# Kernel tuning notes

Hardware: AMD Instinct MI355X
Metric: run time of the kernel (lower is better)

Reference implementation:

```python
import jax, jax.numpy as jnp
import numpy as np

B, N, F_IN = 8, 1024, 256
N_HEADS, N_HIDDEN = 8, 32  # out_features=256, is_concat=True -> n_hidden = 256//8
NEG_SLOPE = 0.2


def setup_inputs() -> dict:
    key = jax.random.key(0)
    k1, k2, k3 = jax.random.split(key, 3)
    vertex = jax.random.normal(k1, (B, N, F_IN), dtype=jnp.float32)
    # linear_vert.weight.T  (applied as x @ w_vert)
    w_vert = jax.random.normal(k2, (F_IN, N_HEADS * N_HIDDEN), dtype=jnp.float32) / np.sqrt(F_IN)
    # attn linear: [2*n_hidden] -> 1, no bias; shared across heads
    attn_w = jax.random.normal(k3, (2 * N_HIDDEN,), dtype=jnp.float32) / np.sqrt(2 * N_HIDDEN)
    return {"vertex": vertex, "w_vert": w_vert, "attn_w": attn_w}


def reference(vertex, w_vert, attn_w):
    b, n, _ = vertex.shape
    # g_vertex: [b, n, h, d]
    g = jnp.einsum("bni,io->bno", vertex, w_vert).reshape(b, n, N_HEADS, N_HIDDEN)
    # attn(cat([g_i, g_j])) == g_i . w_src + g_j . w_dst  (cat index i = repeat_interleave half)
    w_src, w_dst = attn_w[:N_HIDDEN], attn_w[N_HIDDEN:]
    s_src = jnp.einsum("bnhd,d->bnh", g, w_src)  # [b, n, h]
    s_dst = jnp.einsum("bnhd,d->bnh", g, w_dst)  # [b, n, h]
    # e[b,i,j,h] = LeakyReLU(s_src[b,i,h] + s_dst[b,j,h])
    e = s_src[:, :, None, :] + s_dst[:, None, :, :]
    e = jnp.where(e >= 0, e, NEG_SLOPE * e)
    # softmax over j (dim=-2 after squeeze in the torch code)
    a = jax.nn.softmax(e, axis=2)  # [b, i, j, h]
    # dropout in eval mode = identity
    out = jnp.einsum("bijh,bjhd->bihd", a, g)  # [b, n, h, d]
    return out.reshape(b, n, N_HEADS * N_HIDDEN)
```

## Files before the change

### kernel.cpp

```cpp
#include <hip/hip_runtime.h>
#include <hip/hip_bf16.h>
#include <math.h>

#define F_IN  256
#define NOUT  256
#define NB    8
#define NN    1024
#define NH    8
#define ND    32
#define NROWS (NB * NN)
#define LOG2E 1.44269504f

typedef __attribute__((ext_vector_type(8))) short bf16x8;
typedef __attribute__((ext_vector_type(4))) float f32x4;

__device__ inline unsigned pk_bf16(float a, float b) {
    union { __hip_bfloat162 h2; unsigned u; } c;
    c.h2 = __float22bfloat162_rn(make_float2(a, b));
    return c.u;
}
__device__ inline unsigned short bf16u(float a) {
    union { __hip_bfloat16 h; unsigned short u; } c;
    c.h = __float2bfloat16(a);
    return c.u;
}
__device__ inline float bf2f(unsigned short u) {
    union { unsigned u; float f; } c;
    c.u = ((unsigned)u) << 16;
    return c.f;
}
__device__ inline void split8(const float4 va, const float4 vb,
                              bf16x8& hi, bf16x8& lo) {
    float f[8] = {va.x, va.y, va.z, va.w, vb.x, vb.y, vb.z, vb.w};
    union { bf16x8 v; unsigned u[4]; } H, L;
    #pragma unroll
    for (int i = 0; i < 4; ++i) {
        unsigned short h0 = bf16u(f[2 * i]);
        unsigned short h1 = bf16u(f[2 * i + 1]);
        H.u[i] = (unsigned)h0 | ((unsigned)h1 << 16);
        L.u[i] = pk_bf16(f[2 * i] - bf2f(h0), f[2 * i + 1] - bf2f(h1));
    }
    hi = H.v; lo = L.v;
}

__global__ __launch_bounds__(256) void w_prep_kernel(
    const float* __restrict__ w_vert,
    unsigned short* __restrict__ wT_hi, unsigned short* __restrict__ wT_lo)
{
    __shared__ float wf[64][68];
    const int t  = threadIdx.x;
    const int kt = (blockIdx.x >> 2) * 64;
    const int nt = (blockIdx.x & 3) * 64;
    #pragma unroll
    for (int q = 0; q < 4; ++q) {
        const int kr = (t >> 4) + 16 * q;
        const int nc = (t & 15) * 4;
        float4 v = *(const float4*)&w_vert[(size_t)(kt + kr) * NOUT + nt + nc];
        wf[kr][nc + 0] = v.x; wf[kr][nc + 1] = v.y;
        wf[kr][nc + 2] = v.z; wf[kr][nc + 3] = v.w;
    }
    __syncthreads();
    const int n = t >> 2, ks = (t & 3) * 16;
    union { unsigned u[8]; } Hs, Ls;
    #pragma unroll
    for (int i = 0; i < 8; ++i) {
        float x0 = wf[ks + 2 * i][n], x1 = wf[ks + 2 * i + 1][n];
        unsigned short h0 = bf16u(x0), h1 = bf16u(x1);
        Hs.u[i] = (unsigned)h0 | ((unsigned)h1 << 16);
        Ls.u[i] = pk_bf16(x0 - bf2f(h0), x1 - bf2f(h1));
    }
    unsigned* ph = (unsigned*)(wT_hi + (size_t)(nt + n) * F_IN + kt + ks);
    unsigned* pl = (unsigned*)(wT_lo + (size_t)(nt + n) * F_IN + kt + ks);
    #pragma unroll
    for (int i = 0; i < 8; ++i) { ph[i] = Hs.u[i]; pl[i] = Ls.u[i]; }
}

__global__ __launch_bounds__(256) void gat_gemm_kernel(
    const float* __restrict__ vertex,
    const unsigned short* __restrict__ wT_hi,
    const unsigned short* __restrict__ wT_lo,
    const float* __restrict__ attn_w, unsigned short* __restrict__ gT,
    float* __restrict__ ssT, float* __restrict__ sdT)
{
    __shared__ f32x4 comb[2][4][64];

    const int t = threadIdx.x, lane = t & 63, wv = t >> 6;
    const int mt = wv & 1, kh = wv >> 1;
    const int il = lane & 15, ql = lane >> 4;
    const int h = blockIdx.x, gr0 = blockIdx.y * 64;
    const int b = gr0 >> 10, bh = b * NH + h;

    const float* arow0 = vertex + (size_t)(gr0 + mt * 32 + il) * F_IN + kh * 128 + ql * 8;
    const float* arow1 = arow0 + 16 * F_IN;
    const unsigned short* b0h = wT_hi + (size_t)(h * 32 + il) * F_IN + kh * 128 + ql * 8;
    const unsigned short* b1h = b0h + 16 * F_IN;
    const unsigned short* b0l = wT_lo + (size_t)(h * 32 + il) * F_IN + kh * 128 + ql * 8;
    const unsigned short* b1l = b0l + 16 * F_IN;

    f32x4 c00 = {0.f, 0.f, 0.f, 0.f}, c01 = c00, c10 = c00, c11 = c00;

    #pragma unroll 2
    for (int kk = 0; kk < 128; kk += 32) {
        float4 a0a = *(const float4*)(arow0 + kk);
        float4 a0b = *(const float4*)(arow0 + kk + 4);
        float4 a1a = *(const float4*)(arow1 + kk);
        float4 a1b = *(const float4*)(arow1 + kk + 4);
        bf16x8 bh0 = *(const bf16x8*)(b0h + kk);
        bf16x8 bh1 = *(const bf16x8*)(b1h + kk);
        bf16x8 bl0 = *(const bf16x8*)(b0l + kk);
        bf16x8 bl1 = *(const bf16x8*)(b1l + kk);

        bf16x8 a0hi, a0lo, a1hi, a1lo;
        split8(a0a, a0b, a0hi, a0lo);
        split8(a1a, a1b, a1hi, a1lo);

        c00 = __builtin_amdgcn_mfma_f32_16x16x32_bf16(a0hi, bh0, c00, 0, 0, 0);
        c01 = __builtin_amdgcn_mfma_f32_16x16x32_bf16(a0hi, bh1, c01, 0, 0, 0);
        c10 = __builtin_amdgcn_mfma_f32_16x16x32_bf16(a1hi, bh0, c10, 0, 0, 0);
        c11 = __builtin_amdgcn_mfma_f32_16x16x32_bf16(a1hi, bh1, c11, 0, 0, 0);
        c00 = __builtin_amdgcn_mfma_f32_16x16x32_bf16(a0lo, bh0, c00, 0, 0, 0);
        c01 = __builtin_amdgcn_mfma_f32_16x16x32_bf16(a0lo, bh1, c01, 0, 0, 0);
        c10 = __builtin_amdgcn_mfma_f32_16x16x32_bf16(a1lo, bh0, c10, 0, 0, 0);
        c11 = __builtin_amdgcn_mfma_f32_16x16x32_bf16(a1lo, bh1, c11, 0, 0, 0);
        c00 = __builtin_amdgcn_mfma_f32_16x16x32_bf16(a0hi, bl0, c00, 0, 0, 0);
        c01 = __builtin_amdgcn_mfma_f32_16x16x32_bf16(a0hi, bl1, c01, 0, 0, 0);
        c10 = __builtin_amdgcn_mfma_f32_16x16x32_bf16(a1hi, bl0, c10, 0, 0, 0);
        c11 = __builtin_amdgcn_mfma_f32_16x16x32_bf16(a1hi, bl1, c11, 0, 0, 0);
    }

    if (kh == 1) {
        comb[mt][0][lane] = c00; comb[mt][1][lane] = c01;
        comb[mt][2][lane] = c10; comb[mt][3][lane] = c11;
    }
    __syncthreads();
    if (kh == 0) {
        c00 = c00 + comb[mt][0][lane]; c01 = c01 + comb[mt][1][lane];
        c10 = c10 + comb[mt][2][lane]; c11 = c11 + comb[mt][3][lane];

        const int j0 = (gr0 & 1023) + mt * 32;
        const float wsv0 = attn_w[il],      wsv1 = attn_w[16 + il];
        const float wdv0 = attn_w[ND + il], wdv1 = attn_w[ND + 16 + il];

        #pragma unroll
        for (int g = 0; g < 2; ++g) {
            f32x4 cA = g ? c10 : c00;
            f32x4 cB = g ? c11 : c01;
            const int jr = j0 + g * 16 + ql * 4;

            unsigned g2[2];
            g2[0] = pk_bf16(cA[0], cA[1]); g2[1] = pk_bf16(cA[2], cA[3]);
            *(uint2*)(gT + ((size_t)(bh * ND) + il) * NN + jr) = *(uint2*)g2;
            g2[0] = pk_bf16(cB[0], cB[1]); g2[1] = pk_bf16(cB[2], cB[3]);
            *(uint2*)(gT + ((size_t)(bh * ND) + 16 + il) * NN + jr) = *(uint2*)g2;

            #pragma unroll
            for (int reg = 0; reg < 4; ++reg) {
                float ps = cA[reg] * wsv0 + cB[reg] * wsv1;
                float pd = cA[reg] * wdv0 + cB[reg] * wdv1;
                #pragma unroll
                for (int off = 1; off < 16; off <<= 1) {
                    ps += __shfl_xor(ps, off);
                    pd += __shfl_xor(pd, off);
                }
                if (il == 0) {
                    ssT[bh * NN + jr + reg] = ps;
                    sdT[bh * NN + jr + reg] = pd;
                }
            }
        }
    }
}

__global__ __launch_bounds__(256) void gat_attn_kernel(
    const unsigned short* __restrict__ gT, const float* __restrict__ ssT,
    const float* __restrict__ sdT, float* __restrict__ out)
{
    __shared__ __align__(16) float Bp[NN];
    __shared__ __align__(16) float Bn[NN];
    __shared__ float red[4];
    __shared__ f32x4 comb[2][6][64];

    const int b = blockIdx.z, h = blockIdx.y, i0 = blockIdx.x * 32;
    const int t = threadIdx.x, lane = t & 63, jq = t >> 6;
    const int il = lane & 15, ql = lane >> 4;
    const int bh = b * NH + h;

    float sdv[4]; float M = -3.0e38f;
    #pragma unroll
    for (int q = 0; q < 4; ++q) {
        sdv[q] = sdT[bh * NN + t + 256 * q];
        M = fmaxf(M, sdv[q]);
    }
    #pragma unroll
    for (int off = 32; off >= 1; off >>= 1)
        M = fmaxf(M, __shfl_xor(M, off));
    if (lane == 0) red[jq] = M;
    __syncthreads();
    M = fmaxf(fmaxf(red[0], red[1]), fmaxf(red[2], red[3]));

    #pragma unroll
    for (int q = 0; q < 4; ++q) {
        Bp[t + 256 * q] = exp2f(sdv[q] * LOG2E);
        Bn[t + 256 * q] = exp2f(0.2f * LOG2E * sdv[q]);
    }
    const float si0 = ssT[bh * NN + i0 + il];
    const float si1 = ssT[bh * NN + i0 + 16 + il];
    float x0 = si0 + M; x0 = fmaxf(x0, 0.2f * x0);
    float x1 = si1 + M; x1 = fmaxf(x1, 0.2f * x1);
    const float mk0 = x0 * LOG2E, mk1 = x1 * LOG2E;
    const float Ap0 = exp2f(fmaf(si0, LOG2E, -mk0));
    const float An0 = exp2f(fmaf(0.2f * si0, LOG2E, -mk0));
    const float T0  = exp2f(-si0 * LOG2E);
    const float Ap1 = exp2f(fmaf(si1, LOG2E, -mk1));
    const float An1 = exp2f(fmaf(0.2f * si1, LOG2E, -mk1));
    const float T1  = exp2f(-si1 * LOG2E);
    __syncthreads();

    const unsigned short* gb0 = gT + ((size_t)(bh * ND) + il) * NN + jq * 256 + ql * 8;
    const unsigned short* gb1 = gb0 + 16 * NN;
    const float* bpq = &Bp[jq * 256 + ql * 8];
    const float* bnq = &Bn[jq * 256 + ql * 8];

    union { bf16x8 v; unsigned u[4]; } ones;
    ones.u[0] = ones.u[1] = ones.u[2] = ones.u[3] = 0x3F803F80u;

    f32x4 c00 = {0.f, 0.f, 0.f, 0.f}, c01 = c00, c10 = c00, c11 = c00;
    f32x4 cs0 = c00, cs1 = c00;

    #pragma unroll 2
    for (int kk = 0; kk < 256; kk += 32) {
        const float4 p0 = *(const float4*)(bpq + kk);
        const float4 p1 = *(const float4*)(bpq + kk + 4);
        const float4 n0 = *(const float4*)(bnq + kk);
        const float4 n1 = *(const float4*)(bnq + kk + 4);
        const bf16x8 bf0 = *(const bf16x8*)(gb0 + kk);
        const bf16x8 bf1 = *(const bf16x8*)(gb1 + kk);

        float pv[8] = {p0.x, p0.y, p0.z, p0.w, p1.x, p1.y, p1.z, p1.w};
        float nv[8] = {n0.x, n0.y, n0.z, n0.w, n1.x, n1.y, n1.z, n1.w};
        float e0[8], e1[8];
        #pragma unroll
        for (int u = 0; u < 8; ++u) {
            const bool cA = pv[u] >= T0;
            e0[u] = (cA ? Ap0 : An0) * (cA ? pv[u] : nv[u]);
            const bool cB = pv[u] >= T1;
            e1[u] = (cB ? Ap1 : An1) * (cB ? pv[u] : nv[u]);
        }

        union { bf16x8 v; unsigned u[4]; } af0, af1;
        #pragma unroll
        for (int u = 0; u < 4; ++u) {
            af0.u[u] = pk_bf16(e0[2 * u], e0[2 * u + 1]);
            af1.u[u] = pk_bf16(e1[2 * u], e1[2 * u + 1]);
        }

        c00 = __builtin_amdgcn_mfma_f32_16x16x32_bf16(af0.v, bf0, c00, 0, 0, 0);
        c01 = __builtin_amdgcn_mfma_f32_16x16x32_bf16(af0.v, bf1, c01, 0, 0, 0);
        cs0 = __builtin_amdgcn_mfma_f32_16x16x32_bf16(af0.v, ones.v, cs0, 0, 0, 0);
        c10 = __builtin_amdgcn_mfma_f32_16x16x32_bf16(af1.v, bf0, c10, 0, 0, 0);
        c11 = __builtin_amdgcn_mfma_f32_16x16x32_bf16(af1.v, bf1, c11, 0, 0, 0);
        cs1 = __builtin_amdgcn_mfma_f32_16x16x32_bf16(af1.v, ones.v, cs1, 0, 0, 0);
    }

    if (jq >= 2) {
        comb[jq - 2][0][lane] = c00; comb[jq - 2][1][lane] = c01;
        comb[jq - 2][2][lane] = c10; comb[jq - 2][3][lane] = c11;
        comb[jq - 2][4][lane] = cs0; comb[jq - 2][5][lane] = cs1;
    }
    __syncthreads();
    if (jq < 2) {
        c00 = c00 + comb[jq][0][lane]; c01 = c01 + comb[jq][1][lane];
        c10 = c10 + comb[jq][2][lane]; c11 = c11 + comb[jq][3][lane];
        cs0 = cs0 + comb[jq][4][lane]; cs1 = cs1 + comb[jq][5][lane];
    }
    __syncthreads();
    if (jq == 1) {
        comb[0][0][lane] = c00; comb[0][1][lane] = c01;
        comb[0][2][lane] = c10; comb[0][3][lane] = c11;
        comb[0][4][lane] = cs0; comb[0][5][lane] = cs1;
    }
    __syncthreads();
    if (jq == 0) {
        c00 = c00 + comb[0][0][lane]; c01 = c01 + comb[0][1][lane];
        c10 = c10 + comb[0][2][lane]; c11 = c11 + comb[0][3][lane];
        cs0 = cs0 + comb[0][4][lane]; cs1 = cs1 + comb[0][5][lane];

        float r0[4], r1[4];
        #pragma unroll
        for (int reg = 0; reg < 4; ++reg) {
            r0[reg] = 1.0f / cs0[reg];
            r1[reg] = 1.0f / cs1[reg];
        }
        float* ob = out + (size_t)(b * NN + i0 + ql * 4) * NOUT + h * ND + il;
        #pragma unroll
        for (int reg = 0; reg < 4; ++reg) {
            ob[reg * NOUT]             = c00[reg] * r0[reg];
            ob[reg * NOUT + 16]        = c01[reg] * r0[reg];
            ob[(16 + reg) * NOUT]      = c10[reg] * r1[reg];
            ob[(16 + reg) * NOUT + 16] = c11[reg] * r1[reg];
        }
    }
}

extern "C" void kernel_launch(void* const* d_in, const int* in_sizes, int n_in,
                              void* d_out, int out_size, void* d_ws, size_t ws_size,
                              hipStream_t stream) {
    (void)in_sizes; (void)n_in; (void)out_size; (void)ws_size;
    const float* vertex = (const float*)d_in[0];
    const float* w_vert = (const float*)d_in[1];
    const float* attn_w = (const float*)d_in[2];
    float* out = (float*)d_out;

    char* ws = (char*)d_ws;
    unsigned short* wT_hi = (unsigned short*)ws;
    unsigned short* wT_lo = (unsigned short*)(ws + (128 << 10));
    unsigned short* gT    = (unsigned short*)(ws + (256 << 10));
    float* ssT = (float*)(ws + (256 << 10) + ((size_t)NB * NH * ND * NN * 2));
    float* sdT = ssT + (size_t)NB * NH * NN;

    w_prep_kernel<<<16, 256, 0, stream>>>(w_vert, wT_hi, wT_lo);
    gat_gemm_kernel<<<dim3(NH, 128), 256, 0, stream>>>(vertex, wT_hi, wT_lo,
                                                       attn_w, gT, ssT, sdT);
    gat_attn_kernel<<<dim3(32, NH, NB), 256, 0, stream>>>(gT, ssT, sdT, out);
}
```

Baseline: 100.6 us.

## Widen attention tile to 64 rows and use max-based LeakyReLU exponent

The attention kernel now processes 64 query rows per block instead of 32. Each loaded gT fragment and each Bp/Bn shared-memory read is reused across four MFMA row tiles, and the block count halves to 1024 on a flattened grid with bh as the fast index. The branchy threshold select is replaced by fmaxf(Ap*p, An*n), which relies on monotonicity of exp to pick the LeakyReLU branch. The cost is more accumulator registers and twice the shared-memory reduction buffer, partly offset by a launch bound requesting 4 blocks per CU.

```diff
diff --git a/kernel.cpp b/kernel.cpp
--- a/kernel.cpp
+++ b/kernel.cpp
@@ -61,18 +61,18 @@
     }
     __syncthreads();
     const int n = t >> 2, ks = (t & 3) * 16;
-    union { unsigned u[8]; } Hs, Ls;
+    unsigned Hs[8], Ls[8];
     #pragma unroll
     for (int i = 0; i < 8; ++i) {
         float x0 = wf[ks + 2 * i][n], x1 = wf[ks + 2 * i + 1][n];
         unsigned short h0 = bf16u(x0), h1 = bf16u(x1);
-        Hs.u[i] = (unsigned)h0 | ((unsigned)h1 << 16);
-        Ls.u[i] = pk_bf16(x0 - bf2f(h0), x1 - bf2f(h1));
+        Hs[i] = (unsigned)h0 | ((unsigned)h1 << 16);
+        Ls[i] = pk_bf16(x0 - bf2f(h0), x1 - bf2f(h1));
     }
     unsigned* ph = (unsigned*)(wT_hi + (size_t)(nt + n) * F_IN + kt + ks);
     unsigned* pl = (unsigned*)(wT_lo + (size_t)(nt + n) * F_IN + kt + ks);
     #pragma unroll
-    for (int i = 0; i < 8; ++i) { ph[i] = Hs.u[i]; pl[i] = Ls.u[i]; }
+    for (int i = 0; i < 8; ++i) { ph[i] = Hs[i]; pl[i] = Ls[i]; }
 }
 
 __global__ __launch_bounds__(256) void gat_gemm_kernel(
@@ -83,7 +83,6 @@
     float* __restrict__ ssT, float* __restrict__ sdT)
 {
     __shared__ f32x4 comb[2][4][64];
-
     const int t = threadIdx.x, lane = t & 63, wv = t >> 6;
     const int mt = wv & 1, kh = wv >> 1;
     const int il = lane & 15, ql = lane >> 4;
@@ -171,19 +170,21 @@
     }
 }
 
-__global__ __launch_bounds__(256) void gat_attn_kernel(
+__global__ __launch_bounds__(256, 4) void gat_attn_kernel(
     const unsigned short* __restrict__ gT, const float* __restrict__ ssT,
     const float* __restrict__ sdT, float* __restrict__ out)
 {
     __shared__ __align__(16) float Bp[NN];
     __shared__ __align__(16) float Bn[NN];
+    __shared__ f32x4 ccomb[2][12][64];
     __shared__ float red[4];
-    __shared__ f32x4 comb[2][6][64];
-
-    const int b = blockIdx.z, h = blockIdx.y, i0 = blockIdx.x * 32;
+
+    const int bid = blockIdx.x;
+    const int bh = bid & 63;
+    const int b = bh >> 3, h = bh & 7;
+    const int i0 = (bid >> 6) * 64;
     const int t = threadIdx.x, lane = t & 63, jq = t >> 6;
     const int il = lane & 15, ql = lane >> 4;
-    const int bh = b * NH + h;
 
     float sdv[4]; float M = -3.0e38f;
     #pragma unroll
@@ -195,37 +196,38 @@
     for (int off = 32; off >= 1; off >>= 1)
         M = fmaxf(M, __shfl_xor(M, off));
     if (lane == 0) red[jq] = M;
-    __syncthreads();
-    M = fmaxf(fmaxf(red[0], red[1]), fmaxf(red[2], red[3]));
-
     #pragma unroll
     for (int q = 0; q < 4; ++q) {
         Bp[t + 256 * q] = exp2f(sdv[q] * LOG2E);
         Bn[t + 256 * q] = exp2f(0.2f * LOG2E * sdv[q]);
     }
-    const float si0 = ssT[bh * NN + i0 + il];
-    const float si1 = ssT[bh * NN + i0 + 16 + il];
-    float x0 = si0 + M; x0 = fmaxf(x0, 0.2f * x0);
-    float x1 = si1 + M; x1 = fmaxf(x1, 0.2f * x1);
-    const float mk0 = x0 * LOG2E, mk1 = x1 * LOG2E;
-    const float Ap0 = exp2f(fmaf(si0, LOG2E, -mk0));
-    const float An0 = exp2f(fmaf(0.2f * si0, LOG2E, -mk0));
-    const float T0  = exp2f(-si0 * LOG2E);
-    const float Ap1 = exp2f(fmaf(si1, LOG2E, -mk1));
-    const float An1 = exp2f(fmaf(0.2f * si1, LOG2E, -mk1));
-    const float T1  = exp2f(-si1 * LOG2E);
-    __syncthreads();
+    __syncthreads();
+    M = fmaxf(fmaxf(red[0], red[1]), fmaxf(red[2], red[3]));
+
+    float Ap[4], An[4];
+    #pragma unroll
+    for (int mt = 0; mt < 4; ++mt) {
+        const float si = ssT[bh * NN + i0 + mt * 16 + il];
+        float x = si + M; x = fmaxf(x, 0.2f * x);
+        const float mk = x * LOG2E;
+        Ap[mt] = exp2f(fmaf(si, LOG2E, -mk));
+        An[mt] = exp2f(fmaf(0.2f * si, LOG2E, -mk));
+    }
 
     const unsigned short* gb0 = gT + ((size_t)(bh * ND) + il) * NN + jq * 256 + ql * 8;
     const unsigned short* gb1 = gb0 + 16 * NN;
-    const float* bpq = &Bp[jq * 256 + ql * 8];
-    const float* bnq = &Bn[jq * 256 + ql * 8];
+    const float* bpq = Bp + jq * 256 + ql * 8;
+    const float* bnq = Bn + jq * 256 + ql * 8;
 
     union { bf16x8 v; unsigned u[4]; } ones;
     ones.u[0] = ones.u[1] = ones.u[2] = ones.u[3] = 0x3F803F80u;
 
-    f32x4 c00 = {0.f, 0.f, 0.f, 0.f}, c01 = c00, c10 = c00, c11 = c00;
-    f32x4 cs0 = c00, cs1 = c00;
+    f32x4 c0[4], c1[4], cs[4];
+    #pragma unroll
+    for (int mt = 0; mt < 4; ++mt) {
+        c0[mt] = (f32x4){0.f, 0.f, 0.f, 0.f};
+        c1[mt] = c0[mt]; cs[mt] = c0[mt];
+    }
 
     #pragma unroll 2
     for (int kk = 0; kk < 256; kk += 32) {
@@ -238,66 +240,64 @@
 
         float pv[8] = {p0.x, p0.y, p0.z, p0.w, p1.x, p1.y, p1.z, p1.w};
         float nv[8] = {n0.x, n0.y, n0.z, n0.w, n1.x, n1.y, n1.z, n1.w};
-        float e0[8], e1[8];
-        #pragma unroll
-        for (int u = 0; u < 8; ++u) {
-            const bool cA = pv[u] >= T0;
-            e0[u] = (cA ? Ap0 : An0) * (cA ? pv[u] : nv[u]);
-            const bool cB = pv[u] >= T1;
-            e1[u] = (cB ? Ap1 : An1) * (cB ? pv[u] : nv[u]);
-        }
-
-        union { bf16x8 v; unsigned u[4]; } af0, af1;
-        #pragma unroll
-        for (int u = 0; u < 4; ++u) {
-            af0.u[u] = pk_bf16(e0[2 * u], e0[2 * u + 1]);
-            af1.u[u] = pk_bf16(e1[2 * u], e1[2 * u + 1]);
-        }
-
-        c00 = __builtin_amdgcn_mfma_f32_16x16x32_bf16(af0.v, bf0, c00, 0, 0, 0);
-        c01 = __builtin_amdgcn_mfma_f32_16x16x32_bf16(af0.v, bf1, c01, 0, 0, 0);
-        cs0 = __builtin_amdgcn_mfma_f32_16x16x32_bf16(af0.v, ones.v, cs0, 0, 0, 0);
-        c10 = __builtin_amdgcn_mfma_f32_16x16x32_bf16(af1.v, bf0, c10, 0, 0, 0);
-        c11 = __builtin_amdgcn_mfma_f32_16x16x32_bf16(af1.v, bf1, c11, 0, 0, 0);
-        cs1 = __builtin_amdgcn_mfma_f32_16x16x32_bf16(af1.v, ones.v, cs1, 0, 0, 0);
+
+        #pragma unroll
+        for (int mt = 0; mt < 4; ++mt) {
+            float e[8];
+            #pragma unroll
+            for (int u = 0; u < 8; ++u)
+                e[u] = fmaxf(Ap[mt] * pv[u], An[mt] * nv[u]);
+            union { bf16x8 v; unsigned u[4]; } af;
+            #pragma unroll
+            for (int u = 0; u < 4; ++u)
+                af.u[u] = pk_bf16(e[2 * u], e[2 * u + 1]);
+            c0[mt] = __builtin_amdgcn_mfma_f32_16x16x32_bf16(af.v, bf0, c0[mt], 0, 0, 0);
+            c1[mt] = __builtin_amdgcn_mfma_f32_16x16x32_bf16(af.v, bf1, c1[mt], 0, 0, 0);
+            cs[mt] = __builtin_amdgcn_mfma_f32_16x16x32_bf16(af.v, ones.v, cs[mt], 0, 0, 0);
+        }
     }
 
     if (jq >= 2) {
-        comb[jq - 2][0][lane] = c00; comb[jq - 2][1][lane] = c01;
-        comb[jq - 2][2][lane] = c10; comb[jq - 2][3][lane] = c11;
-        comb[jq - 2][4][lane] = cs0; comb[jq - 2][5][lane] = cs1;
+        #pragma unroll
+        for (int mt = 0; mt < 4; ++mt) {
+            ccomb[jq - 2][mt * 3 + 0][lane] = c0[mt];
+            ccomb[jq - 2][mt * 3 + 1][lane] = c1[mt];
+            ccomb[jq - 2][mt * 3 + 2][lane] = cs[mt];
+        }
     }
     __syncthreads();
     if (jq < 2) {
-        c00 = c00 + comb[jq][0][lane]; c01 = c01 + comb[jq][1][lane];
-        c10 = c10 + comb[jq][2][lane]; c11 = c11 + comb[jq][3][lane];
-        cs0 = cs0 + comb[jq][4][lane]; cs1 = cs1 + comb[jq][5][lane];
+        #pragma unroll
+        for (int mt = 0; mt < 4; ++mt) {
+            c0[mt] = c0[mt] + ccomb[jq][mt * 3 + 0][lane];
+            c1[mt] = c1[mt] + ccomb[jq][mt * 3 + 1][lane];
+            cs[mt] = cs[mt] + ccomb[jq][mt * 3 + 2][lane];
+        }
     }
     __syncthreads();
     if (jq == 1) {
-        comb[0][0][lane] = c00; comb[0][1][lane] = c01;
-        comb[0][2][lane] = c10; comb[0][3][lane] = c11;
-        comb[0][4][lane] = cs0; comb[0][5][lane] = cs1;
+        #pragma unroll
+        for (int mt = 0; mt < 4; ++mt) {
+            ccomb[0][mt * 3 + 0][lane] = c0[mt];
+            ccomb[0][mt * 3 + 1][lane] = c1[mt];
+            ccomb[0][mt * 3 + 2][lane] = cs[mt];
+        }
     }
     __syncthreads();
     if (jq == 0) {
-        c00 = c00 + comb[0][0][lane]; c01 = c01 + comb[0][1][lane];
-        c10 = c10 + comb[0][2][lane]; c11 = c11 + comb[0][3][lane];
-        cs0 = cs0 + comb[0][4][lane]; cs1 = cs1 + comb[0][5][lane];
-
-        float r0[4], r1[4];
-        #pragma unroll
-        for (int reg = 0; reg < 4; ++reg) {
-            r0[reg] = 1.0f / cs0[reg];
-            r1[reg] = 1.0f / cs1[reg];
-        }
-        float* ob = out + (size_t)(b * NN + i0 + ql * 4) * NOUT + h * ND + il;
-        #pragma unroll
-        for (int reg = 0; reg < 4; ++reg) {
-            ob[reg * NOUT]             = c00[reg] * r0[reg];
-            ob[reg * NOUT + 16]        = c01[reg] * r0[reg];
-            ob[(16 + reg) * NOUT]      = c10[reg] * r1[reg];
-            ob[(16 + reg) * NOUT + 16] = c11[reg] * r1[reg];
+        #pragma unroll
+        for (int mt = 0; mt < 4; ++mt) {
+            c0[mt] = c0[mt] + ccomb[0][mt * 3 + 0][lane];
+            c1[mt] = c1[mt] + ccomb[0][mt * 3 + 1][lane];
+            cs[mt] = cs[mt] + ccomb[0][mt * 3 + 2][lane];
+
+            float* ob = out + (size_t)(b * NN + i0 + mt * 16 + ql * 4) * NOUT + h * ND + il;
+            #pragma unroll
+            for (int reg = 0; reg < 4; ++reg) {
+                const float r = 1.0f / cs[mt][reg];
+                ob[reg * NOUT]      = c0[mt][reg] * r;
+                ob[reg * NOUT + 16] = c1[mt][reg] * r;
+            }
         }
     }
 }
@@ -321,5 +321,5 @@
     w_prep_kernel<<<16, 256, 0, stream>>>(w_vert, wT_hi, wT_lo);
     gat_gemm_kernel<<<dim3(NH, 128), 256, 0, stream>>>(vertex, wT_hi, wT_lo,
                                                        attn_w, gT, ssT, sdT);
-    gat_attn_kernel<<<dim3(32, NH, NB), 256, 0, stream>>>(gT, ssT, sdT, out);
-}
+    gat_attn_kernel<<<1024, 256, 0, stream>>>(gT, ssT, sdT, out);
+}
```

Measured after the change: 96.72 us. -3.8%, faster.
